# Kernel optimization log

Hardware: AMD Instinct MI355X
Metric: run time of the kernel (lower is better)

The kernel has to match this reference:

```python
import jax, jax.numpy as jnp
import numpy as np

L = 12      # num_layers
E = 768     # embed_dim
H = 12      # num_heads
D = E // H  # head_dim = 64
P = 16      # patch size
NPH = 14    # 224 // 16
NPW = 14
FC = 3072   # 4 * embed_dim
NC = 2      # num_classes


def _pos_enc_2d(nph, npw, dim, temperature=10000.0):
    y, x = jnp.meshgrid(jnp.arange(nph, dtype=jnp.float32), jnp.arange(npw, dtype=jnp.float32), indexing='ij')
    omega = jnp.arange(dim // 4, dtype=jnp.float32) / (dim // 4 - 1)
    omega = 1.0 / temperature ** omega
    y = y.reshape(-1)[:, None] * omega[None, :]
    x = x.reshape(-1)[:, None] * omega[None, :]
    return jnp.concatenate([jnp.sin(x), jnp.cos(x), jnp.sin(y), jnp.cos(y)], axis=1)


def _ln(x, g, b, eps=1e-5):
    m = x.mean(-1, keepdims=True)
    v = x.var(-1, keepdims=True)
    return (x - m) / jnp.sqrt(v + eps) * g + b


def setup_inputs() -> dict:
    key = jax.random.key(0)
    ks = iter(jax.random.split(key, 16))
    nk = lambda: next(ks)
    s = 0.02
    return {
        'img': jax.random.normal(nk(), (32, 3, 224, 224), jnp.float32),
        'patch_w': jax.random.normal(nk(), (P * P * 3, E), jnp.float32) * s,
        'patch_b': jnp.zeros((E,), jnp.float32),
        'cls_token': jax.random.uniform(nk(), (1, 1, E), jnp.float32),
        'Wq': jax.random.normal(nk(), (L, E, E), jnp.float32) * s,
        'Wk': jax.random.normal(nk(), (L, E, E), jnp.float32) * s,
        'Wv': jax.random.normal(nk(), (L, E, E), jnp.float32) * s,
        'Wo': jax.random.normal(nk(), (L, E, E), jnp.float32) * s,
        'bo': jnp.zeros((L, E), jnp.float32),
        'ln1_g': jnp.ones((L, E), jnp.float32),
        'ln1_b': jnp.zeros((L, E), jnp.float32),
        'fln_g': jnp.ones((L, E), jnp.float32),
        'fln_b': jnp.zeros((L, E), jnp.float32),
        'fc1_w': jax.random.normal(nk(), (L, E, FC), jnp.float32) * s,
        'fc1_b': jnp.zeros((L, FC), jnp.float32),
        'fc2_w': jax.random.normal(nk(), (L, FC, E), jnp.float32) * s,
        'fc2_b': jnp.zeros((L, E), jnp.float32),
        'ln2_g': jnp.ones((L, E), jnp.float32),
        'ln2_b': jnp.zeros((L, E), jnp.float32),
        'clf_w': jax.random.normal(nk(), (E, NC), jnp.float32) * s,
        'clf_b': jnp.zeros((NC,), jnp.float32),
    }


def reference(img, patch_w, patch_b, cls_token, Wq, Wk, Wv, Wo, bo,
              ln1_g, ln1_b, fln_g, fln_b, fc1_w, fc1_b, fc2_w, fc2_b,
              ln2_g, ln2_b, clf_w, clf_b):
    B = img.shape[0]
    # patchify: b c (h p1) (w p2) -> b (h w) (p1 p2 c)
    x = img.reshape(B, 3, NPH, P, NPW, P).transpose(0, 2, 4, 3, 5, 1).reshape(B, NPH * NPW, P * P * 3)
    tokens = x @ patch_w + patch_b                              # [B, 196, E]
    cls = jnp.broadcast_to(cls_token, (B, 1, E))
    tokens = jnp.concatenate([cls, tokens], axis=1)             # [B, 197, E]
    pos = _pos_enc_2d(NPH, NPW, E)                              # [196, E]
    pos = jnp.concatenate([jnp.zeros((1, E), pos.dtype), pos], axis=0)
    x = tokens + pos[None]
    scale = D ** -0.5

    def block(x, p):
        wq, wk, wv, wo, bo_, g1, b1, gf, bf, w1, bw1, w2, bw2, g2, b2 = p
        S = x.shape[1]
        q = (x @ wq).reshape(B, S, H, D)
        k = (x @ wk).reshape(B, S, H, D)
        v = (x @ wv).reshape(B, S, H, D)
        logits = jnp.einsum('bshd,bthd->bhst', q, k) * scale    # [B,H,S,S]
        attn = jax.nn.softmax(logits, axis=-1)
        o = jnp.einsum('bhst,bthd->bshd', attn, v).reshape(B, S, E)
        o = o @ wo + bo_
        x = _ln(o + x, g1, b1)
        h = _ln(x, gf, bf) @ w1 + bw1
        h = jax.nn.gelu(h, approximate=False)
        h = h @ w2 + bw2
        x = _ln(h + x, g2, b2)
        return x, None

    x, _ = jax.lax.scan(block, x, (Wq, Wk, Wv, Wo, bo, ln1_g, ln1_b, fln_g, fln_b,
                                   fc1_w, fc1_b, fc2_w, fc2_b, ln2_g, ln2_b))
    return x[:, 0] @ clf_w + clf_b
```

## Files before the change

kernel.cpp:

```cpp
#include <hip/hip_runtime.h>


using bf16x8 = __attribute__((ext_vector_type(8))) short;
using f32x4  = __attribute__((ext_vector_type(4))) float;

__device__ __forceinline__ ushort f2bf(float f) {
    unsigned u = __float_as_uint(f);
    u += 0x7FFFu + ((u >> 16) & 1u);
    return (ushort)(u >> 16);
}
__device__ __forceinline__ float bf2f(ushort h) {
    return __uint_as_float((unsigned)h << 16);
}

__device__ __forceinline__ void async_copy16(const ushort* g, ushort* l) {
    __builtin_amdgcn_global_load_lds(
        (const __attribute__((address_space(1))) void*)g,
        (__attribute__((address_space(3))) void*)l, 16, 0, 0);
}

__device__ __forceinline__ void blockReduce2(float& a, float& b, float* sh) {
#pragma unroll
    for (int off = 32; off > 0; off >>= 1) {
        a += __shfl_down(a, off, 64);
        b += __shfl_down(b, off, 64);
    }
    int wave = threadIdx.x >> 6, lane = threadIdx.x & 63;
    __syncthreads();
    if (lane == 0) { sh[wave] = a; sh[4 + wave] = b; }
    __syncthreads();
    a = sh[0] + sh[1] + sh[2] + sh[3];
    b = sh[4] + sh[5] + sh[6] + sh[7];
}

__global__ void transpose_w_k(const float* __restrict__ in, ushort* __restrict__ out,
                              int K, int N) {
    __shared__ float tile[32][33];
    size_t zoff = (size_t)blockIdx.z * K * N;
    in += zoff; out += zoff;
    int n0 = blockIdx.x * 32, k0 = blockIdx.y * 32;
    int tx = threadIdx.x, ty = threadIdx.y;
#pragma unroll
    for (int i = 0; i < 4; i++)
        tile[ty + i * 8][tx] = in[(size_t)(k0 + ty + i * 8) * N + n0 + tx];
    __syncthreads();
#pragma unroll
    for (int i = 0; i < 4; i++)
        out[(size_t)(n0 + ty + i * 8) * K + k0 + tx] = f2bf(tile[tx][ty + i * 8]);
}

__global__ void transpose_v_k(const ushort* __restrict__ v, ushort* __restrict__ vT) {
    __shared__ ushort tile[32][33];
    int z = blockIdx.z, b = z / 12, hh = z % 12;
    int s0 = blockIdx.x * 32, d0 = blockIdx.y * 32;
    int tx = threadIdx.x, ty = threadIdx.y;
#pragma unroll
    for (int i = 0; i < 4; i++) {
        int s = s0 + ty + i * 8;
        tile[ty + i * 8][tx] =
            (s < 197) ? v[((size_t)(b * 197 + s)) * 768 + hh * 64 + d0 + tx] : (ushort)0;
    }
    __syncthreads();
#pragma unroll
    for (int i = 0; i < 4; i++) {
        int d = d0 + ty + i * 8;
        vT[(size_t)z * 64 * 224 + (size_t)d * 224 + s0 + tx] = tile[tx][ty + i * 8];
    }
}

__global__ __launch_bounds__(256) void patchify_k(const float* __restrict__ img,
                                                  ushort* __restrict__ patches) {
    int idx = blockIdx.x * 256 + threadIdx.x;
    int e = idx % 768, pr = idx / 768;
    int b = pr / 196, p = pr % 196;
    int ph = p / 14, pw = p % 14;
    int c = e % 3, pe = e / 3;
    int p1 = pe >> 4, p2 = pe & 15;
    float v = img[((size_t)(b * 3 + c) * 224 + ph * 16 + p1) * 224 + pw * 16 + p2];
    patches[idx] = f2bf(v);
}

__global__ __launch_bounds__(256) void assemble_k(const float* __restrict__ y,
                                                  const float* __restrict__ cls,
                                                  float* __restrict__ x,
                                                  ushort* __restrict__ xb) {
    int idx = blockIdx.x * 256 + threadIdx.x;
    int e = idx % 768, rr = idx / 768;
    int b = rr / 197, s = rr % 197;
    float val;
    if (s == 0) {
        val = cls[e];
    } else {
        int p = s - 1, iy = p / 14, ix = p % 14;
        int j = e % 192, g = e / 192;
        float om = powf(10000.f, -(float)j * (1.0f / 191.0f));
        float arg = ((g & 2) ? (float)iy : (float)ix) * om;
        float pe = (g & 1) ? cosf(arg) : sinf(arg);
        val = y[(size_t)(b * 196 + p) * 768 + e] + pe;
    }
    x[idx] = val;
    xb[idx] = f2bf(val);
}

__global__ __launch_bounds__(256) void ln_kernel(const float* __restrict__ y,
                                                 float* __restrict__ x,
                                                 ushort* __restrict__ xb,
                                                 ushort* __restrict__ xf,
                                                 const float* __restrict__ g1,
                                                 const float* __restrict__ b1,
                                                 const float* __restrict__ gf,
                                                 const float* __restrict__ bfv,
                                                 int doSecond) {
    __shared__ float red[8];
    int row = blockIdx.x, tid = threadIdx.x;
    const float* yr = y + (size_t)row * 768;
    float* xr = x + (size_t)row * 768;
    float v0[3], s = 0.f, ss = 0.f;
#pragma unroll
    for (int i = 0; i < 3; i++) {
        int c = tid + i * 256;
        float t = yr[c] + xr[c];
        v0[i] = t; s += t; ss += t * t;
    }
    blockReduce2(s, ss, red);
    float m = s * (1.f / 768.f);
    float var = ss * (1.f / 768.f) - m * m;
    float rstd = rsqrtf(var + 1e-5f);
    float s2 = 0.f, ss2 = 0.f, w0[3];
#pragma unroll
    for (int i = 0; i < 3; i++) {
        int c = tid + i * 256;
        float xv = (v0[i] - m) * rstd * g1[c] + b1[c];
        w0[i] = xv;
        xr[c] = xv;
        xb[(size_t)row * 768 + c] = f2bf(xv);
        s2 += xv; ss2 += xv * xv;
    }
    if (doSecond) {
        blockReduce2(s2, ss2, red);
        float m2 = s2 * (1.f / 768.f);
        float var2 = ss2 * (1.f / 768.f) - m2 * m2;
        float r2 = rsqrtf(var2 + 1e-5f);
#pragma unroll
        for (int i = 0; i < 3; i++) {
            int c = tid + i * 256;
            xf[(size_t)row * 768 + c] = f2bf((w0[i] - m2) * r2 * gf[c] + bfv[c]);
        }
    }
}

__global__ __launch_bounds__(64) void softmax_k(ushort* __restrict__ logits) {
    int s = blockIdx.x, z = blockIdx.y, lane = threadIdx.x;
    ushort* row = logits + ((size_t)z * 197 + s) * 224;
    float v[4], mx = -1e30f;
#pragma unroll
    for (int i = 0; i < 4; i++) {
        int c = lane + i * 64;
        float t = -1e30f;
        if (c < 197) t = bf2f(row[c]);
        v[i] = t; mx = fmaxf(mx, t);
    }
#pragma unroll
    for (int off = 32; off > 0; off >>= 1) mx = fmaxf(mx, __shfl_xor(mx, off, 64));
    float sum = 0.f;
#pragma unroll
    for (int i = 0; i < 4; i++) {
        int c = lane + i * 64;
        float ev = 0.f;
        if (c < 197) ev = expf(v[i] - mx);
        v[i] = ev; sum += ev;
    }
#pragma unroll
    for (int off = 32; off > 0; off >>= 1) sum += __shfl_xor(sum, off, 64);
    float inv = 1.f / sum;
#pragma unroll
    for (int i = 0; i < 4; i++) {
        int c = lane + i * 64;
        if (c < 224) row[c] = f2bf(c < 197 ? v[i] * inv : 0.f);
    }
}

__global__ __launch_bounds__(256) void classifier_k(const float* __restrict__ x,
                                                    const float* __restrict__ w,
                                                    const float* __restrict__ bias,
                                                    float* __restrict__ out) {
    __shared__ float red[8];
    int b = blockIdx.x, tid = threadIdx.x;
    const float* xr = x + (size_t)b * 197 * 768;
    float s0 = 0.f, s1 = 0.f;
    for (int e = tid; e < 768; e += 256) {
        float xv = xr[e];
        s0 += xv * w[2 * e];
        s1 += xv * w[2 * e + 1];
    }
    blockReduce2(s0, s1, red);
    if (tid == 0) {
        out[2 * b] = s0 + bias[0];
        out[2 * b + 1] = s1 + bias[1];
    }
}

template <int BM, int BN, int MODE, bool BIAS, bool GELU_ACT, bool OUT_BF16>
__global__ __launch_bounds__(256) void gemm_nt(const ushort* __restrict__ Ab, int lda, long long sAz,
                                               const ushort* __restrict__ Bb, int ldb, long long sBz,
                                               void* __restrict__ Cb, int ldc, long long sCz,
                                               const float* __restrict__ bias,
                                               int M, int N, int K, float scale) {
    constexpr int BK = 32;
    constexpr int TM = BM / 32, TN = BN / 32;
    __shared__ __align__(16) ushort As[BM * BK];
    __shared__ __align__(16) ushort Bs[BN * BK];

    int z = blockIdx.z;
    const ushort* A = Ab;
    const ushort* B = Bb;
    char* C = (char*)Cb;
    if (MODE == 0) {
        A += (size_t)z * sAz;
        B += (size_t)z * sBz;
        C += (size_t)z * sCz * (OUT_BF16 ? 2 : 4);
    } else if (MODE == 1) {
        int b = z / 12, hh = z % 12;
        size_t qo = (size_t)(b * 197) * 768 + hh * 64;
        A += qo; B += qo;
        C += (size_t)z * 197 * 224 * 2;
    } else {
        int b = z / 12, hh = z % 12;
        A += (size_t)z * 197 * 224;
        B += (size_t)z * 64 * 224;
        C += ((size_t)(b * 197) * 768 + hh * 64) * 2;
    }

    int tid = threadIdx.x;
    int lane = tid & 63, wave = tid >> 6;
    int wr = wave >> 1, wc = wave & 1;
    int qq = lane >> 4, rr = lane & 15;
    int lrow = lane >> 2, lck = lane & 3;
    int tileM = blockIdx.y * BM, tileN = blockIdx.x * BN;

    f32x4 acc[TM][TN] = {};

    for (int k0 = 0; k0 < K; k0 += BK) {
#pragma unroll
        for (int it = 0; it < BM / 64; it++) {
            int base_row = (it * 4 + wave) * 16;
            int gr = tileM + base_row + lrow;
            if (gr >= M) gr = M - 1;
            async_copy16(A + (size_t)gr * lda + k0 + lck * 8, As + base_row * BK);
        }
#pragma unroll
        for (int it = 0; it < BN / 64; it++) {
            int base_row = (it * 4 + wave) * 16;
            int gr = tileN + base_row + lrow;
            if (gr >= N) gr = N - 1;
            async_copy16(B + (size_t)gr * ldb + k0 + lck * 8, Bs + base_row * BK);
        }
        __syncthreads();
        bf16x8 af[TM], bfr[TN];
#pragma unroll
        for (int i = 0; i < TM; i++)
            af[i] = *(const bf16x8*)(&As[(wr * TM * 16 + i * 16 + rr) * BK + qq * 8]);
#pragma unroll
        for (int j = 0; j < TN; j++)
            bfr[j] = *(const bf16x8*)(&Bs[(wc * TN * 16 + j * 16 + rr) * BK + qq * 8]);
#pragma unroll
        for (int i = 0; i < TM; i++)
#pragma unroll
            for (int j = 0; j < TN; j++)
                acc[i][j] = __builtin_amdgcn_mfma_f32_16x16x32_bf16(af[i], bfr[j], acc[i][j], 0, 0, 0);
        __syncthreads();
    }

#pragma unroll
    for (int i = 0; i < TM; i++) {
        int rowb = tileM + wr * TM * 16 + i * 16 + qq * 4;
#pragma unroll
        for (int j = 0; j < TN; j++) {
            int colg = tileN + wc * TN * 16 + j * 16 + rr;
            if (colg >= N) continue;
            float bv = BIAS ? bias[colg] : 0.0f;
#pragma unroll
            for (int rg = 0; rg < 4; rg++) {
                int rowg = rowb + rg;
                if (rowg >= M) continue;
                float c = acc[i][j][rg] * scale + bv;
                if (GELU_ACT) c = 0.5f * c * (1.0f + erff(c * 0.70710678118654752f));
                if (OUT_BF16)
                    ((ushort*)C)[(size_t)rowg * ldc + colg] = f2bf(c);
                else
                    ((float*)C)[(size_t)rowg * ldc + colg] = c;
            }
        }
    }
}


extern "C" void kernel_launch(void* const* d_in, const int* in_sizes, int n_in,
                              void* d_out, int out_size, void* d_ws, size_t ws_size,
                              hipStream_t stream) {
    const float* img     = (const float*)d_in[0];
    const float* patch_w = (const float*)d_in[1];
    const float* patch_b = (const float*)d_in[2];
    const float* cls_tok = (const float*)d_in[3];
    const float* Wq      = (const float*)d_in[4];
    const float* Wk      = (const float*)d_in[5];
    const float* Wv      = (const float*)d_in[6];
    const float* Wo      = (const float*)d_in[7];
    const float* bo      = (const float*)d_in[8];
    const float* ln1_g   = (const float*)d_in[9];
    const float* ln1_b   = (const float*)d_in[10];
    const float* fln_g   = (const float*)d_in[11];
    const float* fln_b   = (const float*)d_in[12];
    const float* fc1_w   = (const float*)d_in[13];
    const float* fc1_b   = (const float*)d_in[14];
    const float* fc2_w   = (const float*)d_in[15];
    const float* fc2_b   = (const float*)d_in[16];
    const float* ln2_g   = (const float*)d_in[17];
    const float* ln2_b   = (const float*)d_in[18];
    const float* clf_w   = (const float*)d_in[19];
    const float* clf_b   = (const float*)d_in[20];

    const size_t EE = (size_t)768 * 768;
    const int MROWS = 32 * 197;

    char* ws = (char*)d_ws;
    size_t off = 0;
    auto alloc = [&](size_t bytes) { size_t o = off; off += (bytes + 255) & ~(size_t)255; return o; };
    size_t o_wT     = alloc(48 * EE * 2);
    size_t o_patchT = alloc(EE * 2);
    size_t o_fc1T   = alloc((size_t)12 * 768 * 3072 * 2);
    size_t o_fc2T   = alloc((size_t)12 * 768 * 3072 * 2);
    size_t o_patch  = alloc((size_t)6272 * 768 * 2);
    size_t o_x      = alloc((size_t)MROWS * 768 * 4);
    size_t o_xb     = alloc((size_t)MROWS * 768 * 2);
    size_t o_xf     = alloc((size_t)MROWS * 768 * 2);
    size_t o_qkv    = alloc((size_t)3 * MROWS * 768 * 2);
    size_t o_y      = alloc((size_t)MROWS * 768 * 4);
    size_t o_o      = alloc((size_t)MROWS * 768 * 2);
    size_t logitsB  = (size_t)384 * 197 * 224 * 2;
    size_t vTB      = (size_t)384 * 64 * 224 * 2;
    size_t hB       = (size_t)MROWS * 3072 * 2;
    size_t unionB   = (logitsB + vTB > hB) ? logitsB + vTB : hB;
    size_t o_attn   = alloc(unionB);
    if (off > ws_size) return;

    ushort* wT     = (ushort*)(ws + o_wT);
    ushort* patchT = (ushort*)(ws + o_patchT);
    ushort* fc1T   = (ushort*)(ws + o_fc1T);
    ushort* fc2T   = (ushort*)(ws + o_fc2T);
    ushort* patches= (ushort*)(ws + o_patch);
    float*  x      = (float*)(ws + o_x);
    ushort* xb     = (ushort*)(ws + o_xb);
    ushort* xf     = (ushort*)(ws + o_xf);
    ushort* qkv    = (ushort*)(ws + o_qkv);
    float*  y      = (float*)(ws + o_y);
    ushort* o_     = (ushort*)(ws + o_o);
    ushort* logits = (ushort*)(ws + o_attn);
    ushort* vT     = (ushort*)(ws + o_attn + logitsB);
    ushort* h      = (ushort*)(ws + o_attn);

    dim3 tb(32, 8);
    transpose_w_k<<<dim3(24, 24, 1),  tb, 0, stream>>>(patch_w, patchT, 768, 768);
    transpose_w_k<<<dim3(24, 24, 12), tb, 0, stream>>>(Wq, wT + 0 * 12 * EE, 768, 768);
    transpose_w_k<<<dim3(24, 24, 12), tb, 0, stream>>>(Wk, wT + 1 * 12 * EE, 768, 768);
    transpose_w_k<<<dim3(24, 24, 12), tb, 0, stream>>>(Wv, wT + 2 * 12 * EE, 768, 768);
    transpose_w_k<<<dim3(24, 24, 12), tb, 0, stream>>>(Wo, wT + 3 * 12 * EE, 768, 768);
    transpose_w_k<<<dim3(96, 24, 12), tb, 0, stream>>>(fc1_w, fc1T, 768, 3072);
    transpose_w_k<<<dim3(24, 96, 12), tb, 0, stream>>>(fc2_w, fc2T, 3072, 768);

    patchify_k<<<18816, 256, 0, stream>>>(img, patches);
    gemm_nt<128, 128, 0, true, false, false><<<dim3(6, 49, 1), 256, 0, stream>>>(
        patches, 768, 0, patchT, 768, 0, y, 768, 0, patch_b, 6272, 768, 768, 1.0f);
    assemble_k<<<18912, 256, 0, stream>>>(y, cls_tok, x, xb);

    for (int l = 0; l < 12; ++l) {
        gemm_nt<128, 128, 0, false, false, true><<<dim3(6, 50, 3), 256, 0, stream>>>(
            xb, 768, 0, wT + (size_t)l * EE, 768, (long long)(12 * EE),
            qkv, 768, (long long)MROWS * 768, nullptr, MROWS, 768, 768, 1.0f);
        transpose_v_k<<<dim3(7, 2, 384), tb, 0, stream>>>(qkv + (size_t)2 * MROWS * 768, vT);
        gemm_nt<64, 64, 1, false, false, true><<<dim3(4, 4, 384), 256, 0, stream>>>(
            qkv, 768, 0, qkv + (size_t)MROWS * 768, 768, 0,
            logits, 224, 0, nullptr, 197, 197, 64, 0.125f);
        softmax_k<<<dim3(197, 384), 64, 0, stream>>>(logits);
        gemm_nt<64, 64, 2, false, false, true><<<dim3(1, 4, 384), 256, 0, stream>>>(
            logits, 224, 0, vT, 224, 0, o_, 768, 0, nullptr, 197, 64, 224, 1.0f);
        gemm_nt<128, 128, 0, true, false, false><<<dim3(6, 50, 1), 256, 0, stream>>>(
            o_, 768, 0, wT + (size_t)(36 + l) * EE, 768, 0,
            y, 768, 0, bo + l * 768, MROWS, 768, 768, 1.0f);
        ln_kernel<<<MROWS, 256, 0, stream>>>(y, x, xb, xf, ln1_g + l * 768, ln1_b + l * 768,
                                             fln_g + l * 768, fln_b + l * 768, 1);
        gemm_nt<128, 128, 0, true, true, true><<<dim3(24, 50, 1), 256, 0, stream>>>(
            xf, 768, 0, fc1T + (size_t)l * 768 * 3072, 768, 0,
            h, 3072, 0, fc1_b + l * 3072, MROWS, 3072, 768, 1.0f);
        gemm_nt<128, 128, 0, true, false, false><<<dim3(6, 50, 1), 256, 0, stream>>>(
            h, 3072, 0, fc2T + (size_t)l * 768 * 3072, 3072, 0,
            y, 768, 0, fc2_b + l * 768, MROWS, 768, 3072, 1.0f);
        ln_kernel<<<MROWS, 256, 0, stream>>>(y, x, xb, nullptr, ln2_g + l * 768, ln2_b + l * 768,
                                             nullptr, nullptr, 0);
    }

    classifier_k<<<32, 256, 0, stream>>>(x, clf_w, clf_b, (float*)d_out);
}
```

Before: 4.700 ms.

## Split-K the Wo and fc2 GEMMs and reduce partials inside layernorm

Adds a split-K GEMM mode that writes each K-slice's fp32 partial result to a separate buffer. The Wo projection is split 2-way and fc2 3-way. The following layernorm kernel sums the partials, the bias and the residual before normalizing. The goal is to fill more CUs on these narrow N=768 GEMMs (300 tiles), in exchange for extra fp32 partial traffic and reuse of scratch buffers (qkv and attention regions) for the partials.

```diff
diff --git a/kernel.cpp b/kernel.cpp
--- a/kernel.cpp
+++ b/kernel.cpp
@@ -3,6 +3,8 @@
 
 using bf16x8 = __attribute__((ext_vector_type(8))) short;
 using f32x4  = __attribute__((ext_vector_type(4))) float;
+
+struct CPtrs { void* p[3]; };
 
 __device__ __forceinline__ ushort f2bf(float f) {
     unsigned u = __float_as_uint(f);
@@ -102,24 +104,29 @@
     xb[idx] = f2bf(val);
 }
 
-__global__ __launch_bounds__(256) void ln_kernel(const float* __restrict__ y,
+template <int NP, bool SECOND, bool WXB>
+__global__ __launch_bounds__(256) void ln_kernel(const float* __restrict__ y0,
+                                                 const float* __restrict__ y1,
+                                                 const float* __restrict__ y2,
+                                                 const float* __restrict__ gb,
                                                  float* __restrict__ x,
                                                  ushort* __restrict__ xb,
                                                  ushort* __restrict__ xf,
                                                  const float* __restrict__ g1,
                                                  const float* __restrict__ b1,
                                                  const float* __restrict__ gf,
-                                                 const float* __restrict__ bfv,
-                                                 int doSecond) {
+                                                 const float* __restrict__ bfv) {
     __shared__ float red[8];
     int row = blockIdx.x, tid = threadIdx.x;
-    const float* yr = y + (size_t)row * 768;
-    float* xr = x + (size_t)row * 768;
+    size_t base = (size_t)row * 768;
+    float* xr = x + base;
     float v0[3], s = 0.f, ss = 0.f;
 #pragma unroll
     for (int i = 0; i < 3; i++) {
         int c = tid + i * 256;
-        float t = yr[c] + xr[c];
+        float t = xr[c] + gb[c] + y0[base + c];
+        if (NP > 1) t += y1[base + c];
+        if (NP > 2) t += y2[base + c];
         v0[i] = t; s += t; ss += t * t;
     }
     blockReduce2(s, ss, red);
@@ -133,10 +140,10 @@
         float xv = (v0[i] - m) * rstd * g1[c] + b1[c];
         w0[i] = xv;
         xr[c] = xv;
-        xb[(size_t)row * 768 + c] = f2bf(xv);
+        if (WXB) xb[base + c] = f2bf(xv);
         s2 += xv; ss2 += xv * xv;
     }
-    if (doSecond) {
+    if (SECOND) {
         blockReduce2(s2, ss2, red);
         float m2 = s2 * (1.f / 768.f);
         float var2 = ss2 * (1.f / 768.f) - m2 * m2;
@@ -144,7 +151,7 @@
 #pragma unroll
         for (int i = 0; i < 3; i++) {
             int c = tid + i * 256;
-            xf[(size_t)row * 768 + c] = f2bf((w0[i] - m2) * r2 * gf[c] + bfv[c]);
+            xf[base + c] = f2bf((w0[i] - m2) * r2 * gf[c] + bfv[c]);
         }
     }
 }
@@ -205,7 +212,7 @@
                                                const ushort* __restrict__ Bb, int ldb, long long sBz,
                                                void* __restrict__ Cb, int ldc, long long sCz,
                                                const float* __restrict__ bias,
-                                               int M, int N, int K, float scale) {
+                                               int M, int N, int K, float scale, CPtrs cps) {
     constexpr int BK = 32;
     constexpr int TM = BM / 32, TN = BN / 32;
     __shared__ __align__(16) ushort As[BM * BK];
@@ -224,11 +231,15 @@
         size_t qo = (size_t)(b * 197) * 768 + hh * 64;
         A += qo; B += qo;
         C += (size_t)z * 197 * 224 * 2;
-    } else {
+    } else if (MODE == 2) {
         int b = z / 12, hh = z % 12;
         A += (size_t)z * 197 * 224;
         B += (size_t)z * 64 * 224;
         C += ((size_t)(b * 197) * 768 + hh * 64) * 2;
+    } else {
+        A += (size_t)z * sAz;
+        B += (size_t)z * sBz;
+        C = (char*)cps.p[z];
     }
 
     int tid = threadIdx.x;
@@ -322,6 +333,7 @@
 
     const size_t EE = (size_t)768 * 768;
     const int MROWS = 32 * 197;
+    const size_t ROWB = (size_t)MROWS * 768;
 
     char* ws = (char*)d_ws;
     size_t off = 0;
@@ -331,15 +343,15 @@
     size_t o_fc1T   = alloc((size_t)12 * 768 * 3072 * 2);
     size_t o_fc2T   = alloc((size_t)12 * 768 * 3072 * 2);
     size_t o_patch  = alloc((size_t)6272 * 768 * 2);
-    size_t o_x      = alloc((size_t)MROWS * 768 * 4);
-    size_t o_xb     = alloc((size_t)MROWS * 768 * 2);
-    size_t o_xf     = alloc((size_t)MROWS * 768 * 2);
-    size_t o_qkv    = alloc((size_t)3 * MROWS * 768 * 2);
-    size_t o_y      = alloc((size_t)MROWS * 768 * 4);
-    size_t o_o      = alloc((size_t)MROWS * 768 * 2);
+    size_t o_x      = alloc(ROWB * 4);
+    size_t o_xb     = alloc(ROWB * 2);
+    size_t o_qkv    = alloc(3 * ROWB * 2);
+    size_t o_xf     = alloc(ROWB * 2);
+    size_t o_o      = alloc(ROWB * 2);
+    size_t o_y      = alloc(ROWB * 4);
     size_t logitsB  = (size_t)384 * 197 * 224 * 2;
     size_t vTB      = (size_t)384 * 64 * 224 * 2;
-    size_t hB       = (size_t)MROWS * 3072 * 2;
+    size_t hB       = 3 * ROWB * 2 * 2;
     size_t unionB   = (logitsB + vTB > hB) ? logitsB + vTB : hB;
     size_t o_attn   = alloc(unionB);
     if (off > ws_size) return;
@@ -358,6 +370,11 @@
     ushort* logits = (ushort*)(ws + o_attn);
     ushort* vT     = (ushort*)(ws + o_attn + logitsB);
     ushort* h      = (ushort*)(ws + o_attn);
+    float* woP1  = (float*)(ws + o_attn);
+    float* fc2P1 = (float*)(ws + o_qkv);
+    float* fc2P2 = (float*)(ws + o_qkv + ROWB * 4);
+
+    CPtrs cN{}; CPtrs cWo{{y, woP1, nullptr}}; CPtrs cF2{{y, fc2P1, fc2P2}};
 
     dim3 tb(32, 8);
     transpose_w_k<<<dim3(24, 24, 1),  tb, 0, stream>>>(patch_w, patchT, 768, 768);
@@ -370,33 +387,35 @@
 
     patchify_k<<<18816, 256, 0, stream>>>(img, patches);
     gemm_nt<128, 128, 0, true, false, false><<<dim3(6, 49, 1), 256, 0, stream>>>(
-        patches, 768, 0, patchT, 768, 0, y, 768, 0, patch_b, 6272, 768, 768, 1.0f);
+        patches, 768, 0, patchT, 768, 0, y, 768, 0, patch_b, 6272, 768, 768, 1.0f, cN);
     assemble_k<<<18912, 256, 0, stream>>>(y, cls_tok, x, xb);
 
     for (int l = 0; l < 12; ++l) {
         gemm_nt<128, 128, 0, false, false, true><<<dim3(6, 50, 3), 256, 0, stream>>>(
             xb, 768, 0, wT + (size_t)l * EE, 768, (long long)(12 * EE),
-            qkv, 768, (long long)MROWS * 768, nullptr, MROWS, 768, 768, 1.0f);
-        transpose_v_k<<<dim3(7, 2, 384), tb, 0, stream>>>(qkv + (size_t)2 * MROWS * 768, vT);
+            qkv, 768, (long long)ROWB, nullptr, MROWS, 768, 768, 1.0f, cN);
+        transpose_v_k<<<dim3(7, 2, 384), tb, 0, stream>>>(qkv + 2 * ROWB, vT);
         gemm_nt<64, 64, 1, false, false, true><<<dim3(4, 4, 384), 256, 0, stream>>>(
-            qkv, 768, 0, qkv + (size_t)MROWS * 768, 768, 0,
-            logits, 224, 0, nullptr, 197, 197, 64, 0.125f);
+            qkv, 768, 0, qkv + ROWB, 768, 0,
+            logits, 224, 0, nullptr, 197, 197, 64, 0.125f, cN);
         softmax_k<<<dim3(197, 384), 64, 0, stream>>>(logits);
         gemm_nt<64, 64, 2, false, false, true><<<dim3(1, 4, 384), 256, 0, stream>>>(
-            logits, 224, 0, vT, 224, 0, o_, 768, 0, nullptr, 197, 64, 224, 1.0f);
-        gemm_nt<128, 128, 0, true, false, false><<<dim3(6, 50, 1), 256, 0, stream>>>(
-            o_, 768, 0, wT + (size_t)(36 + l) * EE, 768, 0,
-            y, 768, 0, bo + l * 768, MROWS, 768, 768, 1.0f);
-        ln_kernel<<<MROWS, 256, 0, stream>>>(y, x, xb, xf, ln1_g + l * 768, ln1_b + l * 768,
-                                             fln_g + l * 768, fln_b + l * 768, 1);
+            logits, 224, 0, vT, 224, 0, o_, 768, 0, nullptr, 197, 64, 224, 1.0f, cN);
+        gemm_nt<128, 128, 3, false, false, false><<<dim3(6, 50, 2), 256, 0, stream>>>(
+            o_, 768, 384, wT + (size_t)(36 + l) * EE, 768, 384,
+            nullptr, 768, 0, nullptr, MROWS, 768, 384, 1.0f, cWo);
+        ln_kernel<2, true, false><<<MROWS, 256, 0, stream>>>(
+            y, woP1, nullptr, bo + l * 768, x, nullptr, xf,
+            ln1_g + l * 768, ln1_b + l * 768, fln_g + l * 768, fln_b + l * 768);
         gemm_nt<128, 128, 0, true, true, true><<<dim3(24, 50, 1), 256, 0, stream>>>(
             xf, 768, 0, fc1T + (size_t)l * 768 * 3072, 768, 0,
-            h, 3072, 0, fc1_b + l * 3072, MROWS, 3072, 768, 1.0f);
-        gemm_nt<128, 128, 0, true, false, false><<<dim3(6, 50, 1), 256, 0, stream>>>(
-            h, 3072, 0, fc2T + (size_t)l * 768 * 3072, 3072, 0,
-            y, 768, 0, fc2_b + l * 768, MROWS, 768, 3072, 1.0f);
-        ln_kernel<<<MROWS, 256, 0, stream>>>(y, x, xb, nullptr, ln2_g + l * 768, ln2_b + l * 768,
-                                             nullptr, nullptr, 0);
+            h, 3072, 0, fc1_b + l * 3072, MROWS, 3072, 768, 1.0f, cN);
+        gemm_nt<128, 128, 3, false, false, false><<<dim3(6, 50, 3), 256, 0, stream>>>(
+            h, 3072, 1024, fc2T + (size_t)l * 768 * 3072, 3072, 1024,
+            nullptr, 768, 0, nullptr, MROWS, 768, 1024, 1.0f, cF2);
+        ln_kernel<3, false, true><<<MROWS, 256, 0, stream>>>(
+            y, fc2P1, fc2P2, fc2_b + l * 768, x, xb, nullptr,
+            ln2_g + l * 768, ln2_b + l * 768, nullptr, nullptr);
     }
 
     classifier_k<<<32, 256, 0, stream>>>(x, clf_w, clf_b, (float*)d_out);
```

Measured after the change: 4.294 ms. -8.6%, faster.
